# Kernel optimization log

Hardware: AMD Instinct MI355X
Metric: run time of the kernel (lower is better)

The kernel has to match this reference:

```python
import jax, jax.numpy as jnp
import numpy as np

IN_F, RED, WID, CLS, T = 700, 256, 4096, 20, 100


def _q4(W):
    # per-tensor symmetric INT4 STE: value is quantized, grad is identity
    scale = jnp.maximum(jnp.abs(W).max() / 7.0, 1e-8)
    return W + jax.lax.stop_gradient(jnp.round(W / scale) * scale - W)


def setup_inputs() -> dict:
    key = jax.random.key(0)
    ks = jax.random.split(key, 12)
    B = 64
    x = jax.random.normal(ks[0], (B, T, IN_F), dtype=jnp.float32)
    latent = jax.random.uniform(ks[1], (T,), dtype=jnp.float32)
    spatial_W = jax.random.normal(ks[2], (RED, IN_F), jnp.float32) / np.sqrt(IN_F)
    spatial_b = jnp.zeros((RED,), jnp.float32)
    conv_W = jax.random.normal(ks[3], (RED, RED, 5), jnp.float32) / np.sqrt(RED * 5)
    conv_b = jnp.zeros((RED,), jnp.float32)
    fc1_W = jax.random.normal(ks[4], (WID, RED), jnp.float32) / np.sqrt(RED)
    fc1_b = jnp.zeros((WID,), jnp.float32)
    fc2_W = jax.random.normal(ks[5], (CLS, WID), jnp.float32) / np.sqrt(WID)
    fc2_b = jnp.zeros((CLS,), jnp.float32)
    gain = jnp.asarray(1.0, jnp.float32)
    return {"x": x, "latent": latent, "spatial_W": spatial_W, "spatial_b": spatial_b,
            "conv_W": conv_W, "conv_b": conv_b, "fc1_W": fc1_W, "fc1_b": fc1_b,
            "fc2_W": fc2_W, "fc2_b": fc2_b, "gain": gain}


def _compute_drive(x, latent, spatial_W, spatial_b, conv_W, conv_b, fc1_W, fc1_b, gain):
    # spatial projection (INT4 STE linear) + relu : (B,T,RED)
    xp = jax.nn.relu(jnp.einsum("btf,rf->btr", x, _q4(spatial_W)) + spatial_b)
    # temporal conv1d over T, padding=2 (same), channels RED->RED
    xc = jax.lax.conv_general_dilated(
        xp.transpose(0, 2, 1), conv_W, window_strides=(1,), padding=[(2, 2)],
        dimension_numbers=("NCH", "OIH", "NCH"))
    conv_out = jax.nn.relu(xc + conv_b[None, :, None]).transpose(0, 2, 1)  # (B,T,RED)
    spatial_act = jax.nn.softplus(jnp.einsum("btr,wr->btw", conv_out, _q4(fc1_W)) + fc1_b)
    return spatial_act * latent[None, :, None] * jnp.abs(gain)  # (B,T,WID)


def reference(x, latent, spatial_W, spatial_b, conv_W, conv_b, fc1_W, fc1_b, fc2_W, fc2_b, gain):
    drive = _compute_drive(x, latent, spatial_W, spatial_b, conv_W, conv_b, fc1_W, fc1_b, gain)
    # Poisson spike sampling with straight-through estimator, then clamp at 1
    pois = jax.random.poisson(jax.random.key(42), jax.lax.stop_gradient(drive)).astype(drive.dtype)
    spikes = drive + jax.lax.stop_gradient(pois - drive)
    spikes = jnp.minimum(spikes, 1.0)
    # decay-weighted temporal reduction over T
    decay = jnp.exp(jnp.linspace(-2.0, 0.0, T)).astype(drive.dtype)
    weighted = jnp.einsum("btw,t->bw", spikes, decay)  # (B,WID)
    # dropout in eval mode = identity
    logits = weighted @ _q4(fc2_W).T + fc2_b  # (B,CLS)
    return (logits, spikes, drive)
```

## Files before the change

kernel.cpp:

```cpp
#include <hip/hip_runtime.h>
#include <stdint.h>

#define B 64
#define T 100
#define IN_F 700
#define RED 256
#define WID 4096
#define CLS 20
#define BT (B*T)
#define NELEM (BT*WID)
#define LOGITS_OFF 0
#define SPIKES_OFF (B*CLS)
#define DRIVE_OFF (SPIKES_OFF + NELEM)

#define WS_SLOTS 0
#define WS_W2Q 16
#define WS_XP  (WS_W2Q + CLS*WID)
#define WS_CO  (WS_XP + BT*RED)
#define WS_WEIGHTED (WS_CO + BT*RED)

#define SC_WST 0
#define SC_W1T (SC_WST + IN_F*RED)
#define SC_CWT (SC_W1T + RED*WID)

__host__ __device__ __forceinline__ uint32_t rotl32(uint32_t v, int r) {
  return (v << r) | (v >> (32 - r));
}

__host__ __device__ __forceinline__ void threefry2x32(uint32_t k0, uint32_t k1,
                                                      uint32_t x0, uint32_t x1,
                                                      uint32_t& o0, uint32_t& o1) {
  uint32_t k2 = k0 ^ k1 ^ 0x1BD11BDAu;
  x0 += k0; x1 += k1;
#define TF_R(r) { x0 += x1; x1 = rotl32(x1, (r)); x1 ^= x0; }
  TF_R(13) TF_R(15) TF_R(26) TF_R(6)
  x0 += k1; x1 += k2 + 1u;
  TF_R(17) TF_R(29) TF_R(16) TF_R(24)
  x0 += k2; x1 += k0 + 2u;
  TF_R(13) TF_R(15) TF_R(26) TF_R(6)
  x0 += k0; x1 += k1 + 3u;
  TF_R(17) TF_R(29) TF_R(16) TF_R(24)
  x0 += k1; x1 += k2 + 4u;
  TF_R(13) TF_R(15) TF_R(26) TF_R(6)
  x0 += k2; x1 += k0 + 5u;
#undef TF_R
  o0 = x0; o1 = x1;
}

__global__ void absmax_kernel(const float* __restrict__ w, int n, uint32_t* slot) {
  __shared__ uint32_t sm[256];
  uint32_t m = 0u;
  for (int i = blockIdx.x * 256 + threadIdx.x; i < n; i += gridDim.x * 256)
    m = max(m, __float_as_uint(fabsf(w[i])));
  sm[threadIdx.x] = m;
  __syncthreads();
  for (int s = 128; s > 0; s >>= 1) {
    if (threadIdx.x < s) sm[threadIdx.x] = max(sm[threadIdx.x], sm[threadIdx.x + s]);
    __syncthreads();
  }
  if (threadIdx.x == 0) atomicMax(slot, sm[0]);
}

__global__ void quant_t_kernel(const float* __restrict__ w, float* __restrict__ qT,
                               int Nn, int Kk, const uint32_t* __restrict__ slot) {
  float s = fmaxf(__uint_as_float(*slot) / 7.0f, 1e-8f);
  int id = blockIdx.x * 256 + threadIdx.x;
  if (id < Nn * Kk) {
    int n = id / Kk, k = id - n * Kk;
    qT[(size_t)k * Nn + n] = rintf(w[id] / s) * s;
  }
}

__global__ void quant_kernel(const float* __restrict__ w, float* __restrict__ q,
                             int n, const uint32_t* __restrict__ slot) {
  float s = fmaxf(__uint_as_float(*slot) / 7.0f, 1e-8f);
  int i = blockIdx.x * 256 + threadIdx.x;
  if (i < n) q[i] = rintf(w[i] / s) * s;
}

__global__ void convw_t_kernel(const float* __restrict__ w, float* __restrict__ wt) {
  int id = blockIdx.x * 256 + threadIdx.x;
  if (id < 256 * 1280) {
    int o = id / 1280, r = id - o * 1280;
    int ic = r / 5, h = r - ic * 5;
    wt[(size_t)((h << 8) + ic) * 256 + o] = w[id];
  }
}

template<int SRCA>
__global__ __launch_bounds__(256, 8)
void gemm32_kernel(const float* __restrict__ A, const float* __restrict__ Bt,
                   const float* __restrict__ bias, float* __restrict__ C,
                   int M, int N, int K) {
  constexpr int MT = 32, NT = 64, TM = 2, TN = 4;
  constexpr int ASR = MT + 4, BSR = NT + 4;
  __shared__ float As[32 * ASR];
  __shared__ float Bs[32 * BSR];
  int tid = threadIdx.x;
  int tx = tid & 15, ty = tid >> 4;
  int m0 = blockIdx.x * MT, n0 = blockIdx.y * NT;
  int am = tid >> 3, ak4 = (tid & 7) << 2;
  float acc[TM * TN];
#pragma unroll
  for (int i = 0; i < TM * TN; ++i) acc[i] = 0.f;

  for (int kt = 0; kt < K; kt += 32) {
    int klen = K - kt; if (klen > 32) klen = 32;
    {
      float4 av = make_float4(0.f, 0.f, 0.f, 0.f);
      if (ak4 < klen) {
        if (SRCA == 0) {
          av = *(const float4*)&A[(size_t)(m0 + am) * K + kt + ak4];
        } else {
          int k = kt + ak4;
          int h = k >> 8, ic = k & 255;
          int bt = m0 + am;
          int b = bt / T, t = bt - b * T;
          int tt = t + h - 2;
          if (tt >= 0 && tt < T)
            av = *(const float4*)&A[((size_t)(b * T + tt)) * RED + ic];
        }
      }
      As[(ak4 + 0) * ASR + am] = av.x;
      As[(ak4 + 1) * ASR + am] = av.y;
      As[(ak4 + 2) * ASR + am] = av.z;
      As[(ak4 + 3) * ASR + am] = av.w;
    }
#pragma unroll
    for (int rep = 0; rep < 2; ++rep) {
      int e = rep * 256 + tid;
      int n4 = (e & 15) << 2, kk = e >> 4;
      float4 v = make_float4(0.f, 0.f, 0.f, 0.f);
      if (kk < klen) v = *(const float4*)&Bt[(size_t)(kt + kk) * N + n0 + n4];
      *(float4*)&Bs[kk * BSR + n4] = v;
    }
    __syncthreads();
    if (klen == 32) {
#pragma unroll
      for (int kk = 0; kk < 32; ++kk) {
        float a[TM], b[TN];
#pragma unroll
        for (int i = 0; i < TM; ++i) a[i] = As[kk * ASR + ty * TM + i];
#pragma unroll
        for (int d = 0; d < TN; ++d) b[d] = Bs[kk * BSR + tx * TN + d];
#pragma unroll
        for (int j = 0; j < TM; ++j)
#pragma unroll
          for (int d = 0; d < TN; ++d)
            acc[j * TN + d] = fmaf(a[j], b[d], acc[j * TN + d]);
      }
    } else {
      for (int kk = 0; kk < klen; ++kk) {
        float a[TM], b[TN];
#pragma unroll
        for (int i = 0; i < TM; ++i) a[i] = As[kk * ASR + ty * TM + i];
#pragma unroll
        for (int d = 0; d < TN; ++d) b[d] = Bs[kk * BSR + tx * TN + d];
#pragma unroll
        for (int j = 0; j < TM; ++j)
#pragma unroll
          for (int d = 0; d < TN; ++d)
            acc[j * TN + d] = fmaf(a[j], b[d], acc[j * TN + d]);
      }
    }
    __syncthreads();
  }

  float bv[TN];
#pragma unroll
  for (int d = 0; d < TN; ++d) bv[d] = bias[n0 + tx * TN + d];
#pragma unroll
  for (int j = 0; j < TM; ++j) {
    int m = m0 + ty * TM + j;
#pragma unroll
    for (int d = 0; d < TN; ++d)
      C[(size_t)m * N + n0 + tx * TN + d] = fmaxf(acc[j * TN + d] + bv[d], 0.0f);
  }
}

__global__ __launch_bounds__(256, 4)
void fc1_kernel(const float* __restrict__ A, const float* __restrict__ Bt,
                const float* __restrict__ bias, const float* __restrict__ latent,
                const float* __restrict__ gain, float* __restrict__ C,
                int K, int N) {
  constexpr int ASR = 132, BSR = 132;
  __shared__ float As[32 * ASR];
  __shared__ float Bs[32 * BSR];
  int tid = threadIdx.x;
  int tx = tid & 15, ty = tid >> 4;
  int wid = (blockIdx.x & 7) * 200 + (blockIdx.x >> 3);
  int bx = wid % 50, by = wid / 50;
  int m0 = bx * 128, n0 = by * 128;
  float2 acc2[32];
#pragma unroll
  for (int i = 0; i < 32; ++i) acc2[i] = make_float2(0.f, 0.f);

  for (int kt = 0; kt < K; kt += 32) {
#pragma unroll
    for (int rep = 0; rep < 4; ++rep) {
      int e = rep * 256 + tid;
      int k4 = (e & 7) << 2, m = e >> 3;
      const float4 v = *(const float4*)&A[(size_t)(m0 + m) * K + kt + k4];
      As[(k4 + 0) * ASR + m] = v.x;
      As[(k4 + 1) * ASR + m] = v.y;
      As[(k4 + 2) * ASR + m] = v.z;
      As[(k4 + 3) * ASR + m] = v.w;
    }
#pragma unroll
    for (int rep = 0; rep < 4; ++rep) {
      int e = rep * 256 + tid;
      int n4 = (e & 31) << 2, kk = e >> 5;
      float4 v = *(const float4*)&Bt[(size_t)(kt + kk) * N + n0 + n4];
      *(float4*)&Bs[kk * BSR + n4] = v;
    }
    __syncthreads();
#pragma unroll
    for (int kk = 0; kk < 32; ++kk) {
      float a[8];
#pragma unroll
      for (int i = 0; i < 8; ++i) a[i] = As[kk * ASR + ty * 8 + i];
      float2 b0 = *(const float2*)&Bs[kk * BSR + tx * 4];
      float2 b1 = *(const float2*)&Bs[kk * BSR + tx * 4 + 2];
      float2 b2 = *(const float2*)&Bs[kk * BSR + 64 + tx * 4];
      float2 b3 = *(const float2*)&Bs[kk * BSR + 64 + tx * 4 + 2];
#pragma unroll
      for (int j = 0; j < 8; ++j) {
        acc2[j * 4 + 0].x = fmaf(a[j], b0.x, acc2[j * 4 + 0].x);
        acc2[j * 4 + 0].y = fmaf(a[j], b0.y, acc2[j * 4 + 0].y);
        acc2[j * 4 + 1].x = fmaf(a[j], b1.x, acc2[j * 4 + 1].x);
        acc2[j * 4 + 1].y = fmaf(a[j], b1.y, acc2[j * 4 + 1].y);
        acc2[j * 4 + 2].x = fmaf(a[j], b2.x, acc2[j * 4 + 2].x);
        acc2[j * 4 + 2].y = fmaf(a[j], b2.y, acc2[j * 4 + 2].y);
        acc2[j * 4 + 3].x = fmaf(a[j], b3.x, acc2[j * 4 + 3].x);
        acc2[j * 4 + 3].y = fmaf(a[j], b3.y, acc2[j * 4 + 3].y);
      }
    }
    __syncthreads();
  }

  float g = fabsf(gain[0]);
  float bv[8];
#pragma unroll
  for (int d = 0; d < 4; ++d) {
    bv[d] = bias[n0 + tx * 4 + d];
    bv[4 + d] = bias[n0 + 64 + tx * 4 + d];
  }
#pragma unroll
  for (int j = 0; j < 8; ++j) {
    int bt = m0 + ty * 8 + j;
    int q = bt / T;
    float lat = latent[bt - q * T];
    float o[8];
    o[0] = acc2[j * 4 + 0].x; o[1] = acc2[j * 4 + 0].y;
    o[2] = acc2[j * 4 + 1].x; o[3] = acc2[j * 4 + 1].y;
    o[4] = acc2[j * 4 + 2].x; o[5] = acc2[j * 4 + 2].y;
    o[6] = acc2[j * 4 + 3].x; o[7] = acc2[j * 4 + 3].y;
#pragma unroll
    for (int d = 0; d < 8; ++d) {
      float v = o[d] + bv[d];
      float e = expf(-fabsf(v));
      float l = log1pf(e);
      float sp = fmaxf(v, 0.0f) + l;
      o[d] = (sp * lat) * g;
    }
    float4 o0 = make_float4(o[0], o[1], o[2], o[3]);
    float4 o1 = make_float4(o[4], o[5], o[6], o[7]);
    *(float4*)&C[(size_t)bt * N + n0 + tx * 4] = o0;
    *(float4*)&C[(size_t)bt * N + n0 + 64 + tx * 4] = o1;
  }
}

__global__ __launch_bounds__(256) void spike_weighted_kernel(float* __restrict__ out,
                                                             float* __restrict__ wt,
                                                             uint32_t k0, uint32_t k1) {
  __shared__ float dec[128];
  int tid = threadIdx.x;
  if (tid < T) {
    float step = 2.0f / 99.0f;
    float a = step * (float)tid;
    dec[tid] = expf(a - 2.0f);
  }
  __syncthreads();
  int b = blockIdx.x >> 2;
  int w = ((blockIdx.x & 3) << 10) + (tid << 2);
  float acc0 = 0.f, acc1 = 0.f, acc2 = 0.f, acc3 = 0.f;
  for (int t = 0; t < T; ++t) {
    uint32_t p = (uint32_t)((b * T + t) * WID + w);
    float4 lam = *(const float4*)&out[DRIVE_OFF + p];
    float s[4];
#pragma unroll
    for (int i = 0; i < 4; ++i) {
      uint32_t y0, y1;
      threefry2x32(k0, k1, 0u, p + i, y0, y1);
      uint32_t bits = y0 ^ y1;
      float u = __uint_as_float((bits >> 9) | 0x3f800000u) - 1.0f;
      float lamv = (i == 0) ? lam.x : (i == 1) ? lam.y : (i == 2) ? lam.z : lam.w;
      s[i] = (lamv > 0.0f && logf(u) > -lamv) ? 1.0f : 0.0f;
    }
    *(float4*)&out[SPIKES_OFF + p] = make_float4(s[0], s[1], s[2], s[3]);
    float d = dec[t];
    acc0 = fmaf(s[0], d, acc0);
    acc1 = fmaf(s[1], d, acc1);
    acc2 = fmaf(s[2], d, acc2);
    acc3 = fmaf(s[3], d, acc3);
  }
  *(float4*)&wt[b * WID + w] = make_float4(acc0, acc1, acc2, acc3);
}

__global__ void logits_kernel(const float* __restrict__ wt,
                              const float* __restrict__ w2,
                              const float* __restrict__ b2,
                              float* __restrict__ out) {
  __shared__ float sm[256];
  int b = blockIdx.x / CLS, c = blockIdx.x - b * CLS;
  const float* wr = wt + (size_t)b * WID;
  const float* w2r = w2 + (size_t)c * WID;
  float p = 0.f;
  for (int w = threadIdx.x; w < WID; w += 256) p = fmaf(wr[w], w2r[w], p);
  sm[threadIdx.x] = p;
  __syncthreads();
  for (int s = 128; s > 0; s >>= 1) {
    if (threadIdx.x < s) sm[threadIdx.x] += sm[threadIdx.x + s];
    __syncthreads();
  }
  if (threadIdx.x == 0) out[LOGITS_OFF + blockIdx.x] = sm[0] + b2[c];
}

extern "C" void kernel_launch(void* const* d_in, const int* in_sizes, int n_in,
                              void* d_out, int out_size, void* d_ws, size_t ws_size,
                              hipStream_t stream) {
  (void)in_sizes; (void)n_in; (void)out_size; (void)ws_size;
  const float* x         = (const float*)d_in[0];
  const float* latent    = (const float*)d_in[1];
  const float* spatial_W = (const float*)d_in[2];
  const float* spatial_b = (const float*)d_in[3];
  const float* conv_W    = (const float*)d_in[4];
  const float* conv_b    = (const float*)d_in[5];
  const float* fc1_W     = (const float*)d_in[6];
  const float* fc1_b     = (const float*)d_in[7];
  const float* fc2_W     = (const float*)d_in[8];
  const float* fc2_b     = (const float*)d_in[9];
  const float* gain      = (const float*)d_in[10];
  float* out = (float*)d_out;
  uint32_t* wsu = (uint32_t*)d_ws;
  float* wsf = (float*)d_ws;
  float* S = out + SPIKES_OFF;

  uint32_t sk0, sk1;
  threefry2x32(0u, 42u, 0u, 1u, sk0, sk1);

  hipMemsetAsync(wsu + WS_SLOTS, 0, 3 * sizeof(uint32_t), stream);
  absmax_kernel<<<64, 256, 0, stream>>>(spatial_W, RED * IN_F, wsu + WS_SLOTS + 0);
  absmax_kernel<<<256, 256, 0, stream>>>(fc1_W, WID * RED, wsu + WS_SLOTS + 1);
  absmax_kernel<<<32, 256, 0, stream>>>(fc2_W, CLS * WID, wsu + WS_SLOTS + 2);

  quant_t_kernel<<<700, 256, 0, stream>>>(spatial_W, S + SC_WST, RED, IN_F, wsu + WS_SLOTS + 0);
  quant_t_kernel<<<4096, 256, 0, stream>>>(fc1_W, S + SC_W1T, WID, RED, wsu + WS_SLOTS + 1);
  quant_kernel<<<320, 256, 0, stream>>>(fc2_W, wsf + WS_W2Q, CLS * WID, wsu + WS_SLOTS + 2);
  convw_t_kernel<<<1280, 256, 0, stream>>>(conv_W, S + SC_CWT);

  gemm32_kernel<0><<<dim3(200, 4), 256, 0, stream>>>(
      x, S + SC_WST, spatial_b, wsf + WS_XP, BT, RED, IN_F);

  gemm32_kernel<1><<<dim3(200, 4), 256, 0, stream>>>(
      wsf + WS_XP, S + SC_CWT, conv_b, wsf + WS_CO, BT, RED, 1280);

  fc1_kernel<<<1600, 256, 0, stream>>>(
      wsf + WS_CO, S + SC_W1T, fc1_b, latent, gain, out + DRIVE_OFF, RED, WID);

  spike_weighted_kernel<<<B * 4, 256, 0, stream>>>(out, wsf + WS_WEIGHTED, sk0, sk1);

  logits_kernel<<<B * CLS, 256, 0, stream>>>(wsf + WS_WEIGHTED, wsf + WS_W2Q, fc2_b, out);
}
```

Baseline: 720.2 us.

## Tile weight quant-transpose through LDS and use packed FP32 FMA in fc1

The quantize-transpose kernel now goes through a padded 32x33 shared-memory tile, so both its reads and its writes are coalesced instead of issuing scattered strided stores. The fc1 GEMM inner loop now loads its A and B fragments as float4 and issues v_pk_fma_f32 inline asm with op_sel to broadcast one A element across two accumulators. This is meant to halve the FMA instruction count and cut LDS load instructions. Inline asm can constrain register allocation and scheduling by the compiler.

```diff
diff --git a/kernel.cpp b/kernel.cpp
--- a/kernel.cpp
+++ b/kernel.cpp
@@ -47,6 +47,15 @@
   o0 = x0; o1 = x1;
 }
 
+__device__ __forceinline__ void pk_fma_lo(float2& d, const float2& a, const float2& b) {
+  asm("v_pk_fma_f32 %0, %1, %2, %0 op_sel:[0,0,0] op_sel_hi:[0,1,1]"
+      : "+v"(d) : "v"(a), "v"(b));
+}
+__device__ __forceinline__ void pk_fma_hi(float2& d, const float2& a, const float2& b) {
+  asm("v_pk_fma_f32 %0, %1, %2, %0 op_sel:[1,0,0] op_sel_hi:[1,1,1]"
+      : "+v"(d) : "v"(a), "v"(b));
+}
+
 __global__ void absmax_kernel(const float* __restrict__ w, int n, uint32_t* slot) {
   __shared__ uint32_t sm[256];
   uint32_t m = 0u;
@@ -61,13 +70,26 @@
   if (threadIdx.x == 0) atomicMax(slot, sm[0]);
 }
 
-__global__ void quant_t_kernel(const float* __restrict__ w, float* __restrict__ qT,
-                               int Nn, int Kk, const uint32_t* __restrict__ slot) {
+__global__ __launch_bounds__(256)
+void quant_t_kernel(const float* __restrict__ w, float* __restrict__ qT,
+                    int Nn, int Kk, const uint32_t* __restrict__ slot) {
+  __shared__ float tile[32][33];
   float s = fmaxf(__uint_as_float(*slot) / 7.0f, 1e-8f);
-  int id = blockIdx.x * 256 + threadIdx.x;
-  if (id < Nn * Kk) {
-    int n = id / Kk, k = id - n * Kk;
-    qT[(size_t)k * Nn + n] = rintf(w[id] / s) * s;
+  int tx = threadIdx.x & 31, ty = threadIdx.x >> 5;
+  int k0 = blockIdx.x * 32, n0 = blockIdx.y * 32;
+#pragma unroll
+  for (int r = 0; r < 32; r += 8) {
+    int n = n0 + ty + r, k = k0 + tx;
+    if (n < Nn && k < Kk) {
+      float v = w[(size_t)n * Kk + k];
+      tile[ty + r][tx] = rintf(v / s) * s;
+    }
+  }
+  __syncthreads();
+#pragma unroll
+  for (int r = 0; r < 32; r += 8) {
+    int k = k0 + ty + r, n = n0 + tx;
+    if (k < Kk && n < Nn) qT[(size_t)k * Nn + n] = tile[tx][ty + r];
   }
 }
 
@@ -216,24 +238,26 @@
     __syncthreads();
 #pragma unroll
     for (int kk = 0; kk < 32; ++kk) {
-      float a[8];
-#pragma unroll
-      for (int i = 0; i < 8; ++i) a[i] = As[kk * ASR + ty * 8 + i];
-      float2 b0 = *(const float2*)&Bs[kk * BSR + tx * 4];
-      float2 b1 = *(const float2*)&Bs[kk * BSR + tx * 4 + 2];
-      float2 b2 = *(const float2*)&Bs[kk * BSR + 64 + tx * 4];
-      float2 b3 = *(const float2*)&Bs[kk * BSR + 64 + tx * 4 + 2];
-#pragma unroll
-      for (int j = 0; j < 8; ++j) {
-        acc2[j * 4 + 0].x = fmaf(a[j], b0.x, acc2[j * 4 + 0].x);
-        acc2[j * 4 + 0].y = fmaf(a[j], b0.y, acc2[j * 4 + 0].y);
-        acc2[j * 4 + 1].x = fmaf(a[j], b1.x, acc2[j * 4 + 1].x);
-        acc2[j * 4 + 1].y = fmaf(a[j], b1.y, acc2[j * 4 + 1].y);
-        acc2[j * 4 + 2].x = fmaf(a[j], b2.x, acc2[j * 4 + 2].x);
-        acc2[j * 4 + 2].y = fmaf(a[j], b2.y, acc2[j * 4 + 2].y);
-        acc2[j * 4 + 3].x = fmaf(a[j], b3.x, acc2[j * 4 + 3].x);
-        acc2[j * 4 + 3].y = fmaf(a[j], b3.y, acc2[j * 4 + 3].y);
-      }
+      float4 A0 = *(const float4*)&As[kk * ASR + ty * 8];
+      float4 A1 = *(const float4*)&As[kk * ASR + ty * 8 + 4];
+      float4 B0 = *(const float4*)&Bs[kk * BSR + tx * 4];
+      float4 B1 = *(const float4*)&Bs[kk * BSR + 64 + tx * 4];
+      float2 b0 = make_float2(B0.x, B0.y), b1 = make_float2(B0.z, B0.w);
+      float2 b2 = make_float2(B1.x, B1.y), b3 = make_float2(B1.z, B1.w);
+      float2 a01 = make_float2(A0.x, A0.y), a23 = make_float2(A0.z, A0.w);
+      float2 a45 = make_float2(A1.x, A1.y), a67 = make_float2(A1.z, A1.w);
+#define ROW_LO(j, ap) \
+      pk_fma_lo(acc2[(j)*4+0], ap, b0); pk_fma_lo(acc2[(j)*4+1], ap, b1); \
+      pk_fma_lo(acc2[(j)*4+2], ap, b2); pk_fma_lo(acc2[(j)*4+3], ap, b3);
+#define ROW_HI(j, ap) \
+      pk_fma_hi(acc2[(j)*4+0], ap, b0); pk_fma_hi(acc2[(j)*4+1], ap, b1); \
+      pk_fma_hi(acc2[(j)*4+2], ap, b2); pk_fma_hi(acc2[(j)*4+3], ap, b3);
+      ROW_LO(0, a01) ROW_HI(1, a01)
+      ROW_LO(2, a23) ROW_HI(3, a23)
+      ROW_LO(4, a45) ROW_HI(5, a45)
+      ROW_LO(6, a67) ROW_HI(7, a67)
+#undef ROW_LO
+#undef ROW_HI
     }
     __syncthreads();
   }
@@ -354,8 +378,8 @@
   absmax_kernel<<<256, 256, 0, stream>>>(fc1_W, WID * RED, wsu + WS_SLOTS + 1);
   absmax_kernel<<<32, 256, 0, stream>>>(fc2_W, CLS * WID, wsu + WS_SLOTS + 2);
 
-  quant_t_kernel<<<700, 256, 0, stream>>>(spatial_W, S + SC_WST, RED, IN_F, wsu + WS_SLOTS + 0);
-  quant_t_kernel<<<4096, 256, 0, stream>>>(fc1_W, S + SC_W1T, WID, RED, wsu + WS_SLOTS + 1);
+  quant_t_kernel<<<dim3(22, 8), 256, 0, stream>>>(spatial_W, S + SC_WST, RED, IN_F, wsu + WS_SLOTS + 0);
+  quant_t_kernel<<<dim3(8, 128), 256, 0, stream>>>(fc1_W, S + SC_W1T, WID, RED, wsu + WS_SLOTS + 1);
   quant_kernel<<<320, 256, 0, stream>>>(fc2_W, wsf + WS_W2Q, CLS * WID, wsu + WS_SLOTS + 2);
   convw_t_kernel<<<1280, 256, 0, stream>>>(conv_W, S + SC_CWT);
 
```

Result: slower. 828.5 us (+15.0%).
